# Kernel tuning notes

Measured on AMD Instinct MI355X. Metric: run time of the kernel, lower is better.

The kernel has to match this reference:

```python
import jax, jax.numpy as jnp
import numpy as np

# LIFParameters(thr=0.4, tau=20.0, tau_o=20.0, damp=0.3, n_ref=5)
THR = 0.4
DECAY = float(np.exp(-1.0 / 20.0))   # membrane decay
KAPPA = float(np.exp(-1.0 / 20.0))   # output filter decay
N_REF = 5.0
DAMP = 0.3
SCALE = 1.0                           # scaling_factor

B, NIN, H, NOUT = 1024, 2048, 2048, 512


def setup_inputs() -> dict:
    key = jax.random.key(0)
    ks = jax.random.split(key, 10)
    inputs = (jax.random.uniform(ks[0], (B, NIN)) < 0.1).astype(jnp.float32)   # input spikes
    v = jax.random.uniform(ks[1], (B, H)) * THR                                # membrane potentials
    z = (jax.random.uniform(ks[2], (B, H)) < 0.2).astype(jnp.float32)          # previous spikes
    r = jax.random.randint(ks[3], (B, H), 0, 6).astype(jnp.float32)            # refractory counters
    out = jax.random.normal(ks[4], (B, NOUT)) * 0.1                            # filtered output
    trace_in = jax.random.uniform(ks[5], (B, NIN))
    trace_rec = jax.random.uniform(ks[6], (B, H))
    w_in = jax.random.normal(ks[7], (NIN, H)) / np.sqrt(NIN)
    w_rec = jax.random.normal(ks[8], (H, H)) / np.sqrt(H)
    w_out = jax.random.normal(ks[9], (H, NOUT)) / np.sqrt(H)
    return dict(inputs=inputs, v=v, z=z, r=r, out=out, trace_in=trace_in,
                trace_rec=trace_rec, w_in=w_in, w_rec=w_rec, w_out=w_out)


@jax.custom_vjp
def spike(v_scaled):
    return (v_scaled > 0.0).astype(v_scaled.dtype)

def _spike_fwd(v_scaled):
    return spike(v_scaled), v_scaled

def _spike_bwd(v_scaled, g):
    # surrogate gradient: damp * max(0, 1 - |v_scaled|)
    return (g * DAMP * jnp.maximum(1.0 - jnp.abs(v_scaled), 0.0),)

spike.defvjp(_spike_fwd, _spike_bwd)


def reference(inputs, v, z, r, out, trace_in, trace_rec, w_in, w_rec, w_out):
    # --- lif_step ---
    i_t = inputs @ w_in + z @ w_rec                      # [B,H] synaptic current
    new_v = DECAY * v + i_t - z * THR                    # leaky integration + reset
    v_scaled = (new_v - THR) / THR
    new_z = spike(v_scaled)
    new_z = jnp.where(r > 0.1, 0.0, new_z)               # refractory masking (old r)
    new_r = jnp.clip(r + N_REF * new_z - 1.0, 0.0, N_REF)
    new_out = KAPPA * out + new_z @ (w_out * SCALE)      # [B,NOUT]
    # --- e-prop extras (call_eprop) ---
    dz_dh = jnp.maximum(DAMP * (1.0 - jnp.abs(v_scaled)), 0.0) / THR
    dz_dh = jnp.where(r > 0.1, 0.0, dz_dh)               # zero in refractory period
    new_trace_in = trace_in * DECAY + inputs
    new_trace_rec = trace_rec * DECAY + z
    return (new_out, new_z, new_v, new_r, new_trace_in, new_trace_rec, dz_dh)
```

## Files before the change

### kernel.cpp

```cpp
#include <hip/hip_runtime.h>

#define Bq 1024
#define Hq 2048
#define NOUTq 512

#define DECAYF 0.95122942450071400910f
#define THRF 0.4f

#define OFF_OUT  0
#define OFF_Z    524288
#define OFF_V    2621440
#define OFF_R    4718592
#define OFF_TIN  6815744
#define OFF_TREC 8912896
#define OFF_DZ   11010048

#define WS_ACOMB 0ul
#define WS_WHI   8388608ul
#define WS_WLO   25165824ul
#define WS_WOUTT 41943040ul
#define WS_P     44040192ul
#define WS_Z2    77594624ul
#define WS_NEED  81788928ul

typedef __attribute__((ext_vector_type(8))) short  bf16x8;
typedef __attribute__((ext_vector_type(4))) short  s16x4;
typedef __attribute__((ext_vector_type(4))) float  f32x4;

__device__ __forceinline__ unsigned short cvt_bf16(float f) {
  unsigned u = __float_as_uint(f);
  return (unsigned short)((u + 0x7FFFu + ((u >> 16) & 1u)) >> 16);
}

__device__ __forceinline__ void gl_lds16(const void* g, void* l) {
  __builtin_amdgcn_global_load_lds((const __attribute__((address_space(1))) unsigned int*)g,
                                   (__attribute__((address_space(3))) unsigned int*)l, 16, 0, 0);
}


__global__ __launch_bounds__(256)
void trace_convA(const f32x4* __restrict__ tin, const f32x4* __restrict__ ins,
                 const f32x4* __restrict__ trec, const f32x4* __restrict__ zin,
                 f32x4* __restrict__ o1, f32x4* __restrict__ o2, short* __restrict__ Acomb)
{
  const int i = blockIdx.x * 256 + threadIdx.x;
  const f32x4 b = ins[i];
  const f32x4 d = zin[i];
  o1[i] = tin[i] * DECAYF + b;
  o2[i] = trec[i] * DECAYF + d;
  const int e = i * 4, m = e >> 11, k = e & 2047;
  s16x4 ab, zb;
#pragma unroll
  for (int j = 0; j < 4; ++j) { ab[j] = (short)cvt_bf16(b[j]); zb[j] = (short)cvt_bf16(d[j]); }
  *(s16x4*)&Acomb[m * 4096 + k] = ab;
  *(s16x4*)&Acomb[m * 4096 + 2048 + k] = zb;
}

__global__ __launch_bounds__(256)
void convW(const float* __restrict__ w_in, const float* __restrict__ w_rec,
           const float* __restrict__ w_out, short* __restrict__ Whi,
           short* __restrict__ Wlo, short* __restrict__ WoutT)
{
  __shared__ float tile[64][65];
  const int tid = threadIdx.x;
  const int rr = tid >> 4, c4 = (tid & 15) * 4;
  const int bx = blockIdx.x;
  if (bx < 2048) {
    const int k0 = (bx >> 5) * 64, n0 = (bx & 31) * 64;
#pragma unroll
    for (int p = 0; p < 4; ++p) {
      const int kk = p * 16 + rr, kg = k0 + kk;
      const float* src = (kg < 2048) ? &w_in[kg * 2048 + n0 + c4]
                                     : &w_rec[(kg - 2048) * 2048 + n0 + c4];
      const f32x4 v = *(const f32x4*)src;
#pragma unroll
      for (int j = 0; j < 4; ++j) tile[kk][c4 + j] = v[j];
    }
    __syncthreads();
#pragma unroll
    for (int p = 0; p < 4; ++p) {
      const int nn = p * 16 + rr;
      s16x4 hh, ll;
#pragma unroll
      for (int j = 0; j < 4; ++j) {
        const float w = tile[c4 + j][nn];
        const unsigned short h = cvt_bf16(w);
        hh[j] = (short)h;
        ll[j] = (short)cvt_bf16(w - __uint_as_float(((unsigned)h) << 16));
      }
      *(s16x4*)&Whi[(n0 + nn) * 4096 + k0 + c4] = hh;
      *(s16x4*)&Wlo[(n0 + nn) * 4096 + k0 + c4] = ll;
    }
  } else {
    const int b2 = bx - 2048;
    const int k0 = (b2 >> 3) * 64, n0 = (b2 & 7) * 64;
#pragma unroll
    for (int p = 0; p < 4; ++p) {
      const int kk = p * 16 + rr;
      const f32x4 v = *(const f32x4*)&w_out[(k0 + kk) * 512 + n0 + c4];
#pragma unroll
      for (int j = 0; j < 4; ++j) tile[kk][c4 + j] = v[j];
    }
    __syncthreads();
#pragma unroll
    for (int p = 0; p < 4; ++p) {
      const int nn = p * 16 + rr;
      s16x4 hh;
#pragma unroll
      for (int j = 0; j < 4; ++j) hh[j] = (short)cvt_bf16(tile[c4 + j][nn]);
      *(s16x4*)&WoutT[(n0 + nn) * 2048 + k0 + c4] = hh;
    }
  }
}

template<int MODE>
__global__ __launch_bounds__(256, 1)
void gemm_lds(const short* __restrict__ Ag, const short* __restrict__ Whg,
              const short* __restrict__ Wlg, const float* __restrict__ e0,
              float* __restrict__ outp)
{
  constexpr int BM  = MODE == 0 ? 128 : 32;
  constexpr int BN  = MODE == 0 ? 128 : 64;
  constexpr int MR  = MODE == 0 ? 4 : 1;
  constexpr int NR  = MODE == 0 ? 4 : 2;
  constexpr int KT  = MODE == 0 ? 16 : 32;
  constexpr int AK  = MODE == 0 ? 4096 : 2048;
  constexpr int APW = BM / 32;
  constexpr int WPW = BN / 32;

  __shared__ __align__(16) short As[BM * 64];
  __shared__ __align__(16) short Wh[BN * 64];
  __shared__ __align__(16) short Wl[MODE == 0 ? BN * 64 : 8];

  const int tid = threadIdx.x, lane = tid & 63, wv = tid >> 6;
  const int lr = lane & 15, hl = lane >> 4;
  const int rA = lane >> 3, ts = lane & 7;

  int m0, n0, kz;
  if constexpr (MODE == 0) {
    const int bid = blockIdx.x;
    const int swz = (bid & 7) * 64 + (bid >> 3);
    m0 = (swz & 7) * BM;
    n0 = ((swz >> 3) & 15) * BN;
    kz = swz >> 7;
  } else {
    m0 = blockIdx.y * BM; n0 = blockIdx.x * BN; kz = 0;
  }
  const int kb = kz * 1024;
  float* P = (MODE == 0) ? outp + (size_t)kz * (Bq * Hq) : outp;

  const int wm = (wv >> 1) * (MR * 16);
  const int wn = (wv & 1) * (NR * 16);

  f32x4 acc[MR][NR];
#pragma unroll
  for (int mi = 0; mi < MR; ++mi)
#pragma unroll
    for (int ni = 0; ni < NR; ++ni) acc[mi][ni] = (f32x4){0.f, 0.f, 0.f, 0.f};

  auto STAGE = [&](int kt) {
    const int k = kb + kt * 64;
#pragma unroll
    for (int q = 0; q < APW; ++q) {
      const int slot = wv * APW + q;
      const int r = slot * 8 + rA;
      const int s = ts ^ (r & 7);
      gl_lds16(Ag + (m0 + r) * AK + k + s * 8, &As[slot * 512]);
    }
#pragma unroll
    for (int q = 0; q < WPW; ++q) {
      const int slot = wv * WPW + q;
      const int r = slot * 8 + rA;
      const int s = ts ^ (r & 7);
      gl_lds16(Whg + (n0 + r) * AK + k + s * 8, &Wh[slot * 512]);
      if constexpr (MODE == 0)
        gl_lds16(Wlg + (n0 + r) * AK + k + s * 8, &Wl[slot * 512]);
    }
  };

  STAGE(0);
  for (int kt = 0; kt < KT; ++kt) {
    __syncthreads();
#pragma unroll
    for (int ks = 0; ks < 2; ++ks) {
      bf16x8 af[MR];
#pragma unroll
      for (int mi = 0; mi < MR; ++mi) {
        const int r = wm + mi * 16 + lr;
        af[mi] = *(const bf16x8*)&As[r * 64 + (((ks * 4 + hl) ^ (r & 7)) << 3)];
      }
#pragma unroll
      for (int ni = 0; ni < NR; ++ni) {
        const int rn = wn + ni * 16 + lr;
        const int sp = (((ks * 4 + hl) ^ (rn & 7)) << 3);
        const bf16x8 bh = *(const bf16x8*)&Wh[rn * 64 + sp];
#pragma unroll
        for (int mi = 0; mi < MR; ++mi)
          acc[mi][ni] = __builtin_amdgcn_mfma_f32_16x16x32_bf16(af[mi], bh, acc[mi][ni], 0, 0, 0);
        if constexpr (MODE == 0) {
          const bf16x8 bl = *(const bf16x8*)&Wl[rn * 64 + sp];
#pragma unroll
          for (int mi = 0; mi < MR; ++mi)
            acc[mi][ni] = __builtin_amdgcn_mfma_f32_16x16x32_bf16(af[mi], bl, acc[mi][ni], 0, 0, 0);
        }
      }
    }
    __syncthreads();
    if (kt + 1 < KT) STAGE(kt + 1);
  }

#pragma unroll
  for (int mi = 0; mi < MR; ++mi)
#pragma unroll
    for (int ni = 0; ni < NR; ++ni)
#pragma unroll
      for (int j = 0; j < 4; ++j) {
        const int m = m0 + wm + mi * 16 + hl * 4 + j;
        const int n = n0 + wn + ni * 16 + lr;
        if constexpr (MODE == 0) {
          P[m * Hq + n] = acc[mi][ni][j];
        } else {
          const int idx = m * NOUTq + n;
          outp[idx] = DECAYF * e0[idx] + acc[mi][ni][j];
        }
      }
}

__global__ __launch_bounds__(256)
void lif_epi(const f32x4* __restrict__ Pp, const f32x4* __restrict__ vin,
             const f32x4* __restrict__ zin, const f32x4* __restrict__ rin,
             float* __restrict__ dout, short* __restrict__ z2)
{
  const int i = blockIdx.x * 256 + threadIdx.x;
  const f32x4 it = Pp[i] + Pp[i + 524288] + Pp[i + 2 * 524288] + Pp[i + 3 * 524288];
  const f32x4 vo = vin[i], zo = zin[i], ro = rin[i];
  f32x4 nv, nz, nr, dz;
  s16x4 zb;
#pragma unroll
  for (int j = 0; j < 4; ++j) {
    const float v1 = DECAYF * vo[j] + it[j] - zo[j] * THRF;
    const float vs = (v1 - THRF) / THRF;
    const bool refr = ro[j] > 0.1f;
    const float z1 = (refr || !(vs > 0.0f)) ? 0.0f : 1.0f;
    nv[j] = v1; nz[j] = z1;
    nr[j] = fminf(fmaxf(ro[j] + 5.0f * z1 - 1.0f, 0.0f), 5.0f);
    dz[j] = refr ? 0.0f : (fmaxf(0.3f * (1.0f - fabsf(vs)), 0.0f) / THRF);
    zb[j] = (short)cvt_bf16(z1);
  }
  ((f32x4*)(dout + OFF_V))[i] = nv;
  ((f32x4*)(dout + OFF_Z))[i] = nz;
  ((f32x4*)(dout + OFF_R))[i] = nr;
  ((f32x4*)(dout + OFF_DZ))[i] = dz;
  ((s16x4*)z2)[i] = zb;
}


template<int MODE>
__global__ __launch_bounds__(256, 1)
void fb_gemm(const float* __restrict__ A0g, const float* __restrict__ A1g,
             const float* __restrict__ W0g, const float* __restrict__ W1g,
             const float* __restrict__ e0, const float* __restrict__ e1,
             const float* __restrict__ e2, float* __restrict__ dout)
{
  constexpr int BM = (MODE == 0) ? 64 : 32;
  constexpr int BN = (MODE == 0) ? 128 : 64;
  constexpr int BK = 64;
  constexpr int LDA = BK + 8;
  constexpr int MR = (MODE == 0) ? 2 : 1;
  constexpr int NR = (MODE == 0) ? 4 : 2;
  constexpr int WM = MR * 16, WN = NR * 16;
  constexpr int KT = (MODE == 0) ? 64 : 32;
  constexpr int Nmat = (MODE == 0) ? Hq : NOUTq;
  constexpr int QA = BM / 16;
  constexpr int QW = (16 * BN) / 256;
  constexpr int KSH = (MODE == 0) ? 7 : 6;
  constexpr int KSTEP = (MODE == 0) ? 2 : 4;

  __shared__ __align__(16) short As[BM * LDA];
  __shared__ __align__(16) short Wh[BN * LDA];
  __shared__ __align__(16) short Wl[((MODE == 0) ? BN : 1) * LDA];

  const int tid  = threadIdx.x;
  const int lane = tid & 63;
  const int wave = tid >> 6;
  const int lr = lane & 15, hl = lane >> 4;
  const int wmOff = (wave >> 1) * WM;
  const int wnOff = (wave & 1) * WN;
  const int m0 = blockIdx.y * BM;
  const int n0 = blockIdx.x * BN;
  const int arow = tid >> 4, ac4 = tid & 15;
  const int wn = tid & (BN - 1);

  f32x4 aR[QA];
  float wR[QW][4];
  f32x4 acc[MR][NR];
#pragma unroll
  for (int mi = 0; mi < MR; ++mi)
#pragma unroll
    for (int ni = 0; ni < NR; ++ni)
      acc[mi][ni] = (f32x4){0.f, 0.f, 0.f, 0.f};

  auto LOAD = [&](int kt) {
    const float* Ag = A0g; const float* Wg = W0g; int k0 = kt * BK;
    if (MODE == 0 && kt >= 32) { Ag = A1g; Wg = W1g; k0 = (kt - 32) * BK; }
#pragma unroll
    for (int q = 0; q < QA; ++q)
      aR[q] = *(const f32x4*)&Ag[(m0 + arow + q * 16) * 2048 + k0 + ac4 * 4];
#pragma unroll
    for (int p = 0; p < QW; ++p) {
      const int kq = (tid >> KSH) + p * KSTEP;
#pragma unroll
      for (int i = 0; i < 4; ++i)
        wR[p][i] = Wg[(k0 + kq * 4 + i) * Nmat + n0 + wn];
    }
  };

  auto STORE = [&]() {
#pragma unroll
    for (int q = 0; q < QA; ++q) {
      s16x4 hv;
#pragma unroll
      for (int j = 0; j < 4; ++j) hv[j] = (short)cvt_bf16(aR[q][j]);
      *(s16x4*)&As[(arow + q * 16) * LDA + ac4 * 4] = hv;
    }
#pragma unroll
    for (int p = 0; p < QW; ++p) {
      const int kq = (tid >> KSH) + p * KSTEP;
      s16x4 hh, ll;
#pragma unroll
      for (int i = 0; i < 4; ++i) {
        const float w = wR[p][i];
        const unsigned short h = cvt_bf16(w);
        hh[i] = (short)h;
        if (MODE == 0) {
          const float hf = __uint_as_float(((unsigned)h) << 16);
          ll[i] = (short)cvt_bf16(w - hf);
        }
      }
      *(s16x4*)&Wh[wn * LDA + kq * 4] = hh;
      if (MODE == 0) *(s16x4*)&Wl[wn * LDA + kq * 4] = ll;
    }
  };

  LOAD(0);
  for (int kt = 0; kt < KT; ++kt) {
    __syncthreads();
    STORE();
    __syncthreads();
    if (kt + 1 < KT) LOAD(kt + 1);
#pragma unroll
    for (int ks = 0; ks < 2; ++ks) {
      bf16x8 af[MR];
#pragma unroll
      for (int mi = 0; mi < MR; ++mi)
        af[mi] = *(const bf16x8*)&As[(wmOff + mi * 16 + lr) * LDA + ks * 32 + hl * 8];
#pragma unroll
      for (int ni = 0; ni < NR; ++ni) {
        const bf16x8 bh = *(const bf16x8*)&Wh[(wnOff + ni * 16 + lr) * LDA + ks * 32 + hl * 8];
#pragma unroll
        for (int mi = 0; mi < MR; ++mi)
          acc[mi][ni] = __builtin_amdgcn_mfma_f32_16x16x32_bf16(af[mi], bh, acc[mi][ni], 0, 0, 0);
        if (MODE == 0) {
          const bf16x8 bl = *(const bf16x8*)&Wl[(wnOff + ni * 16 + lr) * LDA + ks * 32 + hl * 8];
#pragma unroll
          for (int mi = 0; mi < MR; ++mi)
            acc[mi][ni] = __builtin_amdgcn_mfma_f32_16x16x32_bf16(af[mi], bl, acc[mi][ni], 0, 0, 0);
        }
      }
    }
  }

#pragma unroll
  for (int mi = 0; mi < MR; ++mi) {
#pragma unroll
    for (int ni = 0; ni < NR; ++ni) {
#pragma unroll
      for (int j = 0; j < 4; ++j) {
        const int m = m0 + wmOff + mi * 16 + hl * 4 + j;
        const int n = n0 + wnOff + ni * 16 + lr;
        if (MODE == 0) {
          const int idx = m * Hq + n;
          const float it = acc[mi][ni][j];
          const float vold = e0[idx];
          const float zold = e1[idx];
          const float rold = e2[idx];
          const float nv = DECAYF * vold + it - zold * THRF;
          const float vs = (nv - THRF) / THRF;
          const bool refr = rold > 0.1f;
          const float nz = (refr || !(vs > 0.0f)) ? 0.0f : 1.0f;
          const float nr = fminf(fmaxf(rold + 5.0f * nz - 1.0f, 0.0f), 5.0f);
          const float dz = refr ? 0.0f : (fmaxf(0.3f * (1.0f - fabsf(vs)), 0.0f) / THRF);
          dout[OFF_V + idx] = nv;
          dout[OFF_Z + idx] = nz;
          dout[OFF_R + idx] = nr;
          dout[OFF_DZ + idx] = dz;
        } else {
          const int idx = m * NOUTq + n;
          dout[OFF_OUT + idx] = DECAYF * e0[idx] + acc[mi][ni][j];
        }
      }
    }
  }
}

__global__ __launch_bounds__(256)
void fb_trace(const float4* __restrict__ tin, const float4* __restrict__ ins,
              const float4* __restrict__ trec, const float4* __restrict__ zin,
              float4* __restrict__ o1, float4* __restrict__ o2)
{
  const int n4 = (Bq * 2048) / 4;
  for (int i = blockIdx.x * blockDim.x + threadIdx.x; i < n4; i += gridDim.x * blockDim.x) {
    const float4 a = tin[i], b = ins[i];
    float4 u;
    u.x = a.x * DECAYF + b.x; u.y = a.y * DECAYF + b.y;
    u.z = a.z * DECAYF + b.z; u.w = a.w * DECAYF + b.w;
    o1[i] = u;
    const float4 c = trec[i], d = zin[i];
    float4 w;
    w.x = c.x * DECAYF + d.x; w.y = c.y * DECAYF + d.y;
    w.z = c.z * DECAYF + d.z; w.w = c.w * DECAYF + d.w;
    o2[i] = w;
  }
}

extern "C" void kernel_launch(void* const* d_in, const int* in_sizes, int n_in,
                              void* d_out, int out_size, void* d_ws, size_t ws_size,
                              hipStream_t stream) {
  const float* inputs = (const float*)d_in[0];
  const float* v      = (const float*)d_in[1];
  const float* z      = (const float*)d_in[2];
  const float* r      = (const float*)d_in[3];
  const float* outp   = (const float*)d_in[4];
  const float* tin    = (const float*)d_in[5];
  const float* trec   = (const float*)d_in[6];
  const float* w_in   = (const float*)d_in[7];
  const float* w_rec  = (const float*)d_in[8];
  const float* w_out  = (const float*)d_in[9];
  float* out = (float*)d_out;

  if (ws_size >= WS_NEED) {
    char* ws = (char*)d_ws;
    short* Acomb = (short*)(ws + WS_ACOMB);
    short* Whi   = (short*)(ws + WS_WHI);
    short* Wlo   = (short*)(ws + WS_WLO);
    short* WoutT = (short*)(ws + WS_WOUTT);
    float* P     = (float*)(ws + WS_P);
    short* Z2    = (short*)(ws + WS_Z2);

    trace_convA<<<2048, 256, 0, stream>>>((const f32x4*)tin, (const f32x4*)inputs,
                                          (const f32x4*)trec, (const f32x4*)z,
                                          (f32x4*)(out + OFF_TIN), (f32x4*)(out + OFF_TREC), Acomb);
    convW<<<2304, 256, 0, stream>>>(w_in, w_rec, w_out, Whi, Wlo, WoutT);
    gemm_lds<0><<<512, 256, 0, stream>>>(Acomb, Whi, Wlo, nullptr, P);
    lif_epi<<<2048, 256, 0, stream>>>((const f32x4*)P, (const f32x4*)v, (const f32x4*)z,
                                      (const f32x4*)r, out, Z2);
    gemm_lds<1><<<dim3(8, 32), 256, 0, stream>>>(Z2, WoutT, nullptr, outp, out + OFF_OUT);
  } else {
    fb_trace<<<2048, 256, 0, stream>>>((const float4*)tin, (const float4*)inputs,
                                       (const float4*)trec, (const float4*)z,
                                       (float4*)(out + OFF_TIN), (float4*)(out + OFF_TREC));
    fb_gemm<0><<<dim3(16, 16), 256, 0, stream>>>(inputs, z, w_in, w_rec, v, z, r, out);
    fb_gemm<1><<<dim3(8, 32), 256, 0, stream>>>(out + OFF_Z, nullptr, w_out, nullptr,
                                                outp, nullptr, nullptr, out);
  }
}
```

Measured before the change: 93.63 us.

## Fuse prep kernels and fold LIF epilogue into split-K GEMM via counters

Merges the trace/activation conversion and weight conversion kernels into one launch. Folds the LIF epilogue into the split-K GEMM: each tile increments an atomic counter, and the last of the four K-slices to finish reduces the partials and applies the LIF update. This removes one kernel launch and the separate full pass that re-read the partials. In exchange it adds a memset, threadfences and atomics, and the epilogue work runs only in the last-arriving blocks, which can leave a tail.

```diff
diff --git a/kernel.cpp b/kernel.cpp
--- a/kernel.cpp
+++ b/kernel.cpp
@@ -21,7 +21,8 @@
 #define WS_WOUTT 41943040ul
 #define WS_P     44040192ul
 #define WS_Z2    77594624ul
-#define WS_NEED  81788928ul
+#define WS_CNT   81788928ul
+#define WS_NEED  81793024ul
 
 typedef __attribute__((ext_vector_type(8))) short  bf16x8;
 typedef __attribute__((ext_vector_type(4))) short  s16x4;
@@ -39,34 +40,33 @@
 
 
 __global__ __launch_bounds__(256)
-void trace_convA(const f32x4* __restrict__ tin, const f32x4* __restrict__ ins,
-                 const f32x4* __restrict__ trec, const f32x4* __restrict__ zin,
-                 f32x4* __restrict__ o1, f32x4* __restrict__ o2, short* __restrict__ Acomb)
-{
-  const int i = blockIdx.x * 256 + threadIdx.x;
-  const f32x4 b = ins[i];
-  const f32x4 d = zin[i];
-  o1[i] = tin[i] * DECAYF + b;
-  o2[i] = trec[i] * DECAYF + d;
-  const int e = i * 4, m = e >> 11, k = e & 2047;
-  s16x4 ab, zb;
-#pragma unroll
-  for (int j = 0; j < 4; ++j) { ab[j] = (short)cvt_bf16(b[j]); zb[j] = (short)cvt_bf16(d[j]); }
-  *(s16x4*)&Acomb[m * 4096 + k] = ab;
-  *(s16x4*)&Acomb[m * 4096 + 2048 + k] = zb;
-}
-
-__global__ __launch_bounds__(256)
-void convW(const float* __restrict__ w_in, const float* __restrict__ w_rec,
-           const float* __restrict__ w_out, short* __restrict__ Whi,
-           short* __restrict__ Wlo, short* __restrict__ WoutT)
+void prep(const f32x4* __restrict__ tin, const f32x4* __restrict__ ins,
+          const f32x4* __restrict__ trec, const f32x4* __restrict__ zin,
+          f32x4* __restrict__ o1, f32x4* __restrict__ o2, short* __restrict__ Acomb,
+          const float* __restrict__ w_in, const float* __restrict__ w_rec,
+          const float* __restrict__ w_out, short* __restrict__ Whi,
+          short* __restrict__ Wlo, short* __restrict__ WoutT)
 {
   __shared__ float tile[64][65];
-  const int tid = threadIdx.x;
+  const int bx = blockIdx.x, tid = threadIdx.x;
+  if (bx < 2048) {
+    const int i = bx * 256 + tid;
+    const f32x4 b = ins[i];
+    const f32x4 d = zin[i];
+    o1[i] = tin[i] * DECAYF + b;
+    o2[i] = trec[i] * DECAYF + d;
+    const int e = i * 4, m = e >> 11, k = e & 2047;
+    s16x4 ab, zb;
+#pragma unroll
+    for (int j = 0; j < 4; ++j) { ab[j] = (short)cvt_bf16(b[j]); zb[j] = (short)cvt_bf16(d[j]); }
+    *(s16x4*)&Acomb[m * 4096 + k] = ab;
+    *(s16x4*)&Acomb[m * 4096 + 2048 + k] = zb;
+    return;
+  }
   const int rr = tid >> 4, c4 = (tid & 15) * 4;
-  const int bx = blockIdx.x;
-  if (bx < 2048) {
-    const int k0 = (bx >> 5) * 64, n0 = (bx & 31) * 64;
+  if (bx < 4096) {
+    const int bxx = bx - 2048;
+    const int k0 = (bxx >> 5) * 64, n0 = (bxx & 31) * 64;
 #pragma unroll
     for (int p = 0; p < 4; ++p) {
       const int kk = p * 16 + rr, kg = k0 + kk;
@@ -92,7 +92,7 @@
       *(s16x4*)&Wlo[(n0 + nn) * 4096 + k0 + c4] = ll;
     }
   } else {
-    const int b2 = bx - 2048;
+    const int b2 = bx - 4096;
     const int k0 = (b2 >> 3) * 64, n0 = (b2 & 7) * 64;
 #pragma unroll
     for (int p = 0; p < 4; ++p) {
@@ -117,7 +117,9 @@
 __global__ __launch_bounds__(256, 1)
 void gemm_lds(const short* __restrict__ Ag, const short* __restrict__ Whg,
               const short* __restrict__ Wlg, const float* __restrict__ e0,
-              float* __restrict__ outp)
+              float* outp, unsigned* cnt,
+              const f32x4* __restrict__ vin, const f32x4* __restrict__ zin,
+              const f32x4* __restrict__ rin, float* dout, short* z2)
 {
   constexpr int BM  = MODE == 0 ? 128 : 32;
   constexpr int BN  = MODE == 0 ? 128 : 64;
@@ -131,6 +133,7 @@
   __shared__ __align__(16) short As[BM * 64];
   __shared__ __align__(16) short Wh[BN * 64];
   __shared__ __align__(16) short Wl[MODE == 0 ? BN * 64 : 8];
+  __shared__ unsigned sFin;
 
   const int tid = threadIdx.x, lane = tid & 63, wv = tid >> 6;
   const int lr = lane & 15, hl = lane >> 4;
@@ -224,34 +227,42 @@
           outp[idx] = DECAYF * e0[idx] + acc[mi][ni][j];
         }
       }
-}
-
-__global__ __launch_bounds__(256)
-void lif_epi(const f32x4* __restrict__ Pp, const f32x4* __restrict__ vin,
-             const f32x4* __restrict__ zin, const f32x4* __restrict__ rin,
-             float* __restrict__ dout, short* __restrict__ z2)
-{
-  const int i = blockIdx.x * 256 + threadIdx.x;
-  const f32x4 it = Pp[i] + Pp[i + 524288] + Pp[i + 2 * 524288] + Pp[i + 3 * 524288];
-  const f32x4 vo = vin[i], zo = zin[i], ro = rin[i];
-  f32x4 nv, nz, nr, dz;
-  s16x4 zb;
-#pragma unroll
-  for (int j = 0; j < 4; ++j) {
-    const float v1 = DECAYF * vo[j] + it[j] - zo[j] * THRF;
-    const float vs = (v1 - THRF) / THRF;
-    const bool refr = ro[j] > 0.1f;
-    const float z1 = (refr || !(vs > 0.0f)) ? 0.0f : 1.0f;
-    nv[j] = v1; nz[j] = z1;
-    nr[j] = fminf(fmaxf(ro[j] + 5.0f * z1 - 1.0f, 0.0f), 5.0f);
-    dz[j] = refr ? 0.0f : (fmaxf(0.3f * (1.0f - fabsf(vs)), 0.0f) / THRF);
-    zb[j] = (short)cvt_bf16(z1);
-  }
-  ((f32x4*)(dout + OFF_V))[i] = nv;
-  ((f32x4*)(dout + OFF_Z))[i] = nz;
-  ((f32x4*)(dout + OFF_R))[i] = nr;
-  ((f32x4*)(dout + OFF_DZ))[i] = dz;
-  ((s16x4*)z2)[i] = zb;
+
+  if constexpr (MODE == 0) {
+    __threadfence();
+    const int tileId = (m0 >> 7) * 16 + (n0 >> 7);
+    if (tid == 0) sFin = atomicAdd(cnt + tileId, 1u);
+    __syncthreads();
+    if (sFin == 3u) {
+      __threadfence();
+      const f32x4* P4 = (const f32x4*)outp;
+      const int row4 = n0 >> 2;
+      for (int q = tid; q < (BM * BN) / 4; q += 256) {
+        const int row = q >> 5, c4i = q & 31;
+        const int g4 = (m0 + row) * (Hq / 4) + row4 + c4i;
+        const f32x4 it = P4[g4] + P4[g4 + 524288] + P4[g4 + 2 * 524288] + P4[g4 + 3 * 524288];
+        const f32x4 vo = vin[g4], zo = zin[g4], ro = rin[g4];
+        f32x4 nv, nz, nr, dz;
+        s16x4 zb;
+#pragma unroll
+        for (int j = 0; j < 4; ++j) {
+          const float v1 = DECAYF * vo[j] + it[j] - zo[j] * THRF;
+          const float vs = (v1 - THRF) / THRF;
+          const bool refr = ro[j] > 0.1f;
+          const float z1 = (refr || !(vs > 0.0f)) ? 0.0f : 1.0f;
+          nv[j] = v1; nz[j] = z1;
+          nr[j] = fminf(fmaxf(ro[j] + 5.0f * z1 - 1.0f, 0.0f), 5.0f);
+          dz[j] = refr ? 0.0f : (fmaxf(0.3f * (1.0f - fabsf(vs)), 0.0f) / THRF);
+          zb[j] = (short)cvt_bf16(z1);
+        }
+        ((f32x4*)(dout + OFF_V))[g4] = nv;
+        ((f32x4*)(dout + OFF_Z))[g4] = nz;
+        ((f32x4*)(dout + OFF_R))[g4] = nr;
+        ((f32x4*)(dout + OFF_DZ))[g4] = dz;
+        ((s16x4*)z2)[g4] = zb;
+      }
+    }
+  }
 }
 
 
@@ -446,15 +457,19 @@
     short* WoutT = (short*)(ws + WS_WOUTT);
     float* P     = (float*)(ws + WS_P);
     short* Z2    = (short*)(ws + WS_Z2);
-
-    trace_convA<<<2048, 256, 0, stream>>>((const f32x4*)tin, (const f32x4*)inputs,
-                                          (const f32x4*)trec, (const f32x4*)z,
-                                          (f32x4*)(out + OFF_TIN), (f32x4*)(out + OFF_TREC), Acomb);
-    convW<<<2304, 256, 0, stream>>>(w_in, w_rec, w_out, Whi, Wlo, WoutT);
-    gemm_lds<0><<<512, 256, 0, stream>>>(Acomb, Whi, Wlo, nullptr, P);
-    lif_epi<<<2048, 256, 0, stream>>>((const f32x4*)P, (const f32x4*)v, (const f32x4*)z,
-                                      (const f32x4*)r, out, Z2);
-    gemm_lds<1><<<dim3(8, 32), 256, 0, stream>>>(Z2, WoutT, nullptr, outp, out + OFF_OUT);
+    unsigned* C  = (unsigned*)(ws + WS_CNT);
+
+    hipMemsetAsync(C, 0, 512, stream);
+    prep<<<4352, 256, 0, stream>>>((const f32x4*)tin, (const f32x4*)inputs,
+                                   (const f32x4*)trec, (const f32x4*)z,
+                                   (f32x4*)(out + OFF_TIN), (f32x4*)(out + OFF_TREC), Acomb,
+                                   w_in, w_rec, w_out, Whi, Wlo, WoutT);
+    gemm_lds<0><<<512, 256, 0, stream>>>(Acomb, Whi, Wlo, nullptr, P, C,
+                                         (const f32x4*)v, (const f32x4*)z, (const f32x4*)r,
+                                         out, Z2);
+    gemm_lds<1><<<dim3(8, 32), 256, 0, stream>>>(Z2, WoutT, nullptr, outp, out + OFF_OUT,
+                                                 nullptr, nullptr, nullptr, nullptr,
+                                                 nullptr, nullptr);
   } else {
     fb_trace<<<2048, 256, 0, stream>>>((const float4*)tin, (const float4*)inputs,
                                        (const float4*)trec, (const float4*)z,
```

Result: slower. 218.2 us (+133.1%).

## Merge prep kernels and retile main GEMM to 128x64 with split-K of two

Applied to the files above, without the earlier changes.

Merges the trace/A-conversion kernel and the weight conversion kernel into a single prep launch that dispatches on block index, removing one kernel launch and its tail. The main GEMM now uses 128x64 tiles with a 2-way K split instead of 128x128 tiles with a 4-way split, still with 512 blocks. That halves the partial-sum buffer traffic the LIF epilogue reads and writes. The trade-off is less register-level reuse per block and longer K loops per block.

```diff
diff --git a/kernel.cpp b/kernel.cpp
--- a/kernel.cpp
+++ b/kernel.cpp
@@ -39,34 +39,33 @@
 
 
 __global__ __launch_bounds__(256)
-void trace_convA(const f32x4* __restrict__ tin, const f32x4* __restrict__ ins,
-                 const f32x4* __restrict__ trec, const f32x4* __restrict__ zin,
-                 f32x4* __restrict__ o1, f32x4* __restrict__ o2, short* __restrict__ Acomb)
-{
-  const int i = blockIdx.x * 256 + threadIdx.x;
-  const f32x4 b = ins[i];
-  const f32x4 d = zin[i];
-  o1[i] = tin[i] * DECAYF + b;
-  o2[i] = trec[i] * DECAYF + d;
-  const int e = i * 4, m = e >> 11, k = e & 2047;
-  s16x4 ab, zb;
-#pragma unroll
-  for (int j = 0; j < 4; ++j) { ab[j] = (short)cvt_bf16(b[j]); zb[j] = (short)cvt_bf16(d[j]); }
-  *(s16x4*)&Acomb[m * 4096 + k] = ab;
-  *(s16x4*)&Acomb[m * 4096 + 2048 + k] = zb;
-}
-
-__global__ __launch_bounds__(256)
-void convW(const float* __restrict__ w_in, const float* __restrict__ w_rec,
-           const float* __restrict__ w_out, short* __restrict__ Whi,
-           short* __restrict__ Wlo, short* __restrict__ WoutT)
+void prep(const f32x4* __restrict__ tin, const f32x4* __restrict__ ins,
+          const f32x4* __restrict__ trec, const f32x4* __restrict__ zin,
+          f32x4* __restrict__ o1, f32x4* __restrict__ o2, short* __restrict__ Acomb,
+          const float* __restrict__ w_in, const float* __restrict__ w_rec,
+          const float* __restrict__ w_out, short* __restrict__ Whi,
+          short* __restrict__ Wlo, short* __restrict__ WoutT)
 {
   __shared__ float tile[64][65];
-  const int tid = threadIdx.x;
+  const int bx = blockIdx.x, tid = threadIdx.x;
+  if (bx < 2048) {
+    const int i = bx * 256 + tid;
+    const f32x4 b = ins[i];
+    const f32x4 d = zin[i];
+    o1[i] = tin[i] * DECAYF + b;
+    o2[i] = trec[i] * DECAYF + d;
+    const int e = i * 4, m = e >> 11, k = e & 2047;
+    s16x4 ab, zb;
+#pragma unroll
+    for (int j = 0; j < 4; ++j) { ab[j] = (short)cvt_bf16(b[j]); zb[j] = (short)cvt_bf16(d[j]); }
+    *(s16x4*)&Acomb[m * 4096 + k] = ab;
+    *(s16x4*)&Acomb[m * 4096 + 2048 + k] = zb;
+    return;
+  }
   const int rr = tid >> 4, c4 = (tid & 15) * 4;
-  const int bx = blockIdx.x;
-  if (bx < 2048) {
-    const int k0 = (bx >> 5) * 64, n0 = (bx & 31) * 64;
+  if (bx < 4096) {
+    const int bxx = bx - 2048;
+    const int k0 = (bxx >> 5) * 64, n0 = (bxx & 31) * 64;
 #pragma unroll
     for (int p = 0; p < 4; ++p) {
       const int kk = p * 16 + rr, kg = k0 + kk;
@@ -92,7 +91,7 @@
       *(s16x4*)&Wlo[(n0 + nn) * 4096 + k0 + c4] = ll;
     }
   } else {
-    const int b2 = bx - 2048;
+    const int b2 = bx - 4096;
     const int k0 = (b2 >> 3) * 64, n0 = (b2 & 7) * 64;
 #pragma unroll
     for (int p = 0; p < 4; ++p) {
@@ -120,10 +119,10 @@
               float* __restrict__ outp)
 {
   constexpr int BM  = MODE == 0 ? 128 : 32;
-  constexpr int BN  = MODE == 0 ? 128 : 64;
+  constexpr int BN  = 64;
   constexpr int MR  = MODE == 0 ? 4 : 1;
-  constexpr int NR  = MODE == 0 ? 4 : 2;
-  constexpr int KT  = MODE == 0 ? 16 : 32;
+  constexpr int NR  = 2;
+  constexpr int KT  = 32;
   constexpr int AK  = MODE == 0 ? 4096 : 2048;
   constexpr int APW = BM / 32;
   constexpr int WPW = BN / 32;
@@ -141,12 +140,12 @@
     const int bid = blockIdx.x;
     const int swz = (bid & 7) * 64 + (bid >> 3);
     m0 = (swz & 7) * BM;
-    n0 = ((swz >> 3) & 15) * BN;
-    kz = swz >> 7;
+    n0 = ((swz >> 3) & 31) * BN;
+    kz = swz >> 8;
   } else {
     m0 = blockIdx.y * BM; n0 = blockIdx.x * BN; kz = 0;
   }
-  const int kb = kz * 1024;
+  const int kb = kz * 2048;
   float* P = (MODE == 0) ? outp + (size_t)kz * (Bq * Hq) : outp;
 
   const int wm = (wv >> 1) * (MR * 16);
@@ -232,7 +231,7 @@
              float* __restrict__ dout, short* __restrict__ z2)
 {
   const int i = blockIdx.x * 256 + threadIdx.x;
-  const f32x4 it = Pp[i] + Pp[i + 524288] + Pp[i + 2 * 524288] + Pp[i + 3 * 524288];
+  const f32x4 it = Pp[i] + Pp[i + 524288];
   const f32x4 vo = vin[i], zo = zin[i], ro = rin[i];
   f32x4 nv, nz, nr, dz;
   s16x4 zb;
@@ -447,10 +446,10 @@
     float* P     = (float*)(ws + WS_P);
     short* Z2    = (short*)(ws + WS_Z2);
 
-    trace_convA<<<2048, 256, 0, stream>>>((const f32x4*)tin, (const f32x4*)inputs,
-                                          (const f32x4*)trec, (const f32x4*)z,
-                                          (f32x4*)(out + OFF_TIN), (f32x4*)(out + OFF_TREC), Acomb);
-    convW<<<2304, 256, 0, stream>>>(w_in, w_rec, w_out, Whi, Wlo, WoutT);
+    prep<<<4352, 256, 0, stream>>>((const f32x4*)tin, (const f32x4*)inputs,
+                                   (const f32x4*)trec, (const f32x4*)z,
+                                   (f32x4*)(out + OFF_TIN), (f32x4*)(out + OFF_TREC), Acomb,
+                                   w_in, w_rec, w_out, Whi, Wlo, WoutT);
     gemm_lds<0><<<512, 256, 0, stream>>>(Acomb, Whi, Wlo, nullptr, P);
     lif_epi<<<2048, 256, 0, stream>>>((const f32x4*)P, (const f32x4*)v, (const f32x4*)z,
                                       (const f32x4*)r, out, Z2);
```

After: 92.97 us. About the same (-0.7%).

## Merge activation conversion into weight prep and trace updates into output GEMM

Applied to the files above, without the earlier changes.

Folds the bf16 conversion of inputs and z into the weight-conversion kernel as extra blocks. It also moves the trace_in/trace_rec decay updates into the final output GEMM launch as extra blocks. This removes one launch and lets the elementwise trace work run alongside the small, under-occupied output GEMM instead of serially at the start. The trade-off is that the tail kernel loses the launch_bounds(256,1) hint, and block scheduling order may delay the GEMM blocks.

```diff
diff --git a/kernel.cpp b/kernel.cpp
--- a/kernel.cpp
+++ b/kernel.cpp
@@ -39,32 +39,27 @@
 
 
 __global__ __launch_bounds__(256)
-void trace_convA(const f32x4* __restrict__ tin, const f32x4* __restrict__ ins,
-                 const f32x4* __restrict__ trec, const f32x4* __restrict__ zin,
-                 f32x4* __restrict__ o1, f32x4* __restrict__ o2, short* __restrict__ Acomb)
-{
-  const int i = blockIdx.x * 256 + threadIdx.x;
-  const f32x4 b = ins[i];
-  const f32x4 d = zin[i];
-  o1[i] = tin[i] * DECAYF + b;
-  o2[i] = trec[i] * DECAYF + d;
-  const int e = i * 4, m = e >> 11, k = e & 2047;
-  s16x4 ab, zb;
-#pragma unroll
-  for (int j = 0; j < 4; ++j) { ab[j] = (short)cvt_bf16(b[j]); zb[j] = (short)cvt_bf16(d[j]); }
-  *(s16x4*)&Acomb[m * 4096 + k] = ab;
-  *(s16x4*)&Acomb[m * 4096 + 2048 + k] = zb;
-}
-
-__global__ __launch_bounds__(256)
-void convW(const float* __restrict__ w_in, const float* __restrict__ w_rec,
-           const float* __restrict__ w_out, short* __restrict__ Whi,
-           short* __restrict__ Wlo, short* __restrict__ WoutT)
+void prepWA(const float* __restrict__ w_in, const float* __restrict__ w_rec,
+            const float* __restrict__ w_out, short* __restrict__ Whi,
+            short* __restrict__ Wlo, short* __restrict__ WoutT,
+            const f32x4* __restrict__ ins, const f32x4* __restrict__ zin,
+            short* __restrict__ Acomb)
 {
   __shared__ float tile[64][65];
-  const int tid = threadIdx.x;
+  const int bx = blockIdx.x, tid = threadIdx.x;
+  if (bx >= 2304) {
+    const int i = (bx - 2304) * 256 + tid;
+    const f32x4 b = ins[i];
+    const f32x4 d = zin[i];
+    const int e = i * 4, m = e >> 11, k = e & 2047;
+    s16x4 ab, zb;
+#pragma unroll
+    for (int j = 0; j < 4; ++j) { ab[j] = (short)cvt_bf16(b[j]); zb[j] = (short)cvt_bf16(d[j]); }
+    *(s16x4*)&Acomb[m * 4096 + k] = ab;
+    *(s16x4*)&Acomb[m * 4096 + 2048 + k] = zb;
+    return;
+  }
   const int rr = tid >> 4, c4 = (tid & 15) * 4;
-  const int bx = blockIdx.x;
   if (bx < 2048) {
     const int k0 = (bx >> 5) * 64, n0 = (bx & 31) * 64;
 #pragma unroll
@@ -113,41 +108,28 @@
   }
 }
 
-template<int MODE>
 __global__ __launch_bounds__(256, 1)
-void gemm_lds(const short* __restrict__ Ag, const short* __restrict__ Whg,
-              const short* __restrict__ Wlg, const float* __restrict__ e0,
-              float* __restrict__ outp)
+void gemm1(const short* __restrict__ Ag, const short* __restrict__ Whg,
+           const short* __restrict__ Wlg, float* __restrict__ outp)
 {
-  constexpr int BM  = MODE == 0 ? 128 : 32;
-  constexpr int BN  = MODE == 0 ? 128 : 64;
-  constexpr int MR  = MODE == 0 ? 4 : 1;
-  constexpr int NR  = MODE == 0 ? 4 : 2;
-  constexpr int KT  = MODE == 0 ? 16 : 32;
-  constexpr int AK  = MODE == 0 ? 4096 : 2048;
-  constexpr int APW = BM / 32;
-  constexpr int WPW = BN / 32;
+  constexpr int BM = 128, BN = 128, MR = 4, NR = 4, KT = 16, AK = 4096;
+  constexpr int APW = BM / 32, WPW = BN / 32;
 
   __shared__ __align__(16) short As[BM * 64];
   __shared__ __align__(16) short Wh[BN * 64];
-  __shared__ __align__(16) short Wl[MODE == 0 ? BN * 64 : 8];
+  __shared__ __align__(16) short Wl[BN * 64];
 
   const int tid = threadIdx.x, lane = tid & 63, wv = tid >> 6;
   const int lr = lane & 15, hl = lane >> 4;
   const int rA = lane >> 3, ts = lane & 7;
 
-  int m0, n0, kz;
-  if constexpr (MODE == 0) {
-    const int bid = blockIdx.x;
-    const int swz = (bid & 7) * 64 + (bid >> 3);
-    m0 = (swz & 7) * BM;
-    n0 = ((swz >> 3) & 15) * BN;
-    kz = swz >> 7;
-  } else {
-    m0 = blockIdx.y * BM; n0 = blockIdx.x * BN; kz = 0;
-  }
+  const int bid = blockIdx.x;
+  const int swz = (bid & 7) * 64 + (bid >> 3);
+  const int m0 = (swz & 7) * BM;
+  const int n0 = ((swz >> 3) & 15) * BN;
+  const int kz = swz >> 7;
   const int kb = kz * 1024;
-  float* P = (MODE == 0) ? outp + (size_t)kz * (Bq * Hq) : outp;
+  float* P = outp + (size_t)kz * (Bq * Hq);
 
   const int wm = (wv >> 1) * (MR * 16);
   const int wn = (wv & 1) * (NR * 16);
@@ -173,8 +155,7 @@
       const int r = slot * 8 + rA;
       const int s = ts ^ (r & 7);
       gl_lds16(Whg + (n0 + r) * AK + k + s * 8, &Wh[slot * 512]);
-      if constexpr (MODE == 0)
-        gl_lds16(Wlg + (n0 + r) * AK + k + s * 8, &Wl[slot * 512]);
+      gl_lds16(Wlg + (n0 + r) * AK + k + s * 8, &Wl[slot * 512]);
     }
   };
 
@@ -197,12 +178,10 @@
 #pragma unroll
         for (int mi = 0; mi < MR; ++mi)
           acc[mi][ni] = __builtin_amdgcn_mfma_f32_16x16x32_bf16(af[mi], bh, acc[mi][ni], 0, 0, 0);
-        if constexpr (MODE == 0) {
-          const bf16x8 bl = *(const bf16x8*)&Wl[rn * 64 + sp];
-#pragma unroll
-          for (int mi = 0; mi < MR; ++mi)
-            acc[mi][ni] = __builtin_amdgcn_mfma_f32_16x16x32_bf16(af[mi], bl, acc[mi][ni], 0, 0, 0);
-        }
+        const bf16x8 bl = *(const bf16x8*)&Wl[rn * 64 + sp];
+#pragma unroll
+        for (int mi = 0; mi < MR; ++mi)
+          acc[mi][ni] = __builtin_amdgcn_mfma_f32_16x16x32_bf16(af[mi], bl, acc[mi][ni], 0, 0, 0);
       }
     }
     __syncthreads();
@@ -217,12 +196,7 @@
       for (int j = 0; j < 4; ++j) {
         const int m = m0 + wm + mi * 16 + hl * 4 + j;
         const int n = n0 + wn + ni * 16 + lr;
-        if constexpr (MODE == 0) {
-          P[m * Hq + n] = acc[mi][ni][j];
-        } else {
-          const int idx = m * NOUTq + n;
-          outp[idx] = DECAYF * e0[idx] + acc[mi][ni][j];
-        }
+        P[m * Hq + n] = acc[mi][ni][j];
       }
 }
 
@@ -252,6 +226,94 @@
   ((f32x4*)(dout + OFF_R))[i] = nr;
   ((f32x4*)(dout + OFF_DZ))[i] = dz;
   ((s16x4*)z2)[i] = zb;
+}
+
+__global__ __launch_bounds__(256)
+void tail(const short* __restrict__ Ag, const short* __restrict__ Whg,
+          const float* __restrict__ e0, float* __restrict__ outp,
+          const f32x4* __restrict__ tin, const f32x4* __restrict__ ins,
+          const f32x4* __restrict__ trec, const f32x4* __restrict__ zin,
+          f32x4* __restrict__ o1, f32x4* __restrict__ o2)
+{
+  constexpr int BM = 32, BN = 64, MR = 1, NR = 2, KT = 32, AK = 2048;
+  constexpr int APW = BM / 32, WPW = BN / 32;
+  __shared__ __align__(16) short As[BM * 64];
+  __shared__ __align__(16) short Wh[BN * 64];
+
+  const int bid = blockIdx.x, tid = threadIdx.x;
+  if (bid >= 256) {
+    const int i = (bid - 256) * 256 + tid;
+    o1[i] = tin[i] * DECAYF + ins[i];
+    o2[i] = trec[i] * DECAYF + zin[i];
+    return;
+  }
+  const int lane = tid & 63, wv = tid >> 6;
+  const int lr = lane & 15, hl = lane >> 4;
+  const int rA = lane >> 3, ts = lane & 7;
+  const int m0 = (bid >> 3) * BM, n0 = (bid & 7) * BN;
+  const int wm = (wv >> 1) * (MR * 16);
+  const int wn = (wv & 1) * (NR * 16);
+
+  f32x4 acc[MR][NR];
+#pragma unroll
+  for (int mi = 0; mi < MR; ++mi)
+#pragma unroll
+    for (int ni = 0; ni < NR; ++ni) acc[mi][ni] = (f32x4){0.f, 0.f, 0.f, 0.f};
+
+  auto STAGE = [&](int kt) {
+    const int k = kt * 64;
+#pragma unroll
+    for (int q = 0; q < APW; ++q) {
+      const int slot = wv * APW + q;
+      const int r = slot * 8 + rA;
+      const int s = ts ^ (r & 7);
+      gl_lds16(Ag + (m0 + r) * AK + k + s * 8, &As[slot * 512]);
+    }
+#pragma unroll
+    for (int q = 0; q < WPW; ++q) {
+      const int slot = wv * WPW + q;
+      const int r = slot * 8 + rA;
+      const int s = ts ^ (r & 7);
+      gl_lds16(Whg + (n0 + r) * AK + k + s * 8, &Wh[slot * 512]);
+    }
+  };
+
+  STAGE(0);
+  for (int kt = 0; kt < KT; ++kt) {
+    __syncthreads();
+#pragma unroll
+    for (int ks = 0; ks < 2; ++ks) {
+      bf16x8 af[MR];
+#pragma unroll
+      for (int mi = 0; mi < MR; ++mi) {
+        const int r = wm + mi * 16 + lr;
+        af[mi] = *(const bf16x8*)&As[r * 64 + (((ks * 4 + hl) ^ (r & 7)) << 3)];
+      }
+#pragma unroll
+      for (int ni = 0; ni < NR; ++ni) {
+        const int rn = wn + ni * 16 + lr;
+        const int sp = (((ks * 4 + hl) ^ (rn & 7)) << 3);
+        const bf16x8 bh = *(const bf16x8*)&Wh[rn * 64 + sp];
+#pragma unroll
+        for (int mi = 0; mi < MR; ++mi)
+          acc[mi][ni] = __builtin_amdgcn_mfma_f32_16x16x32_bf16(af[mi], bh, acc[mi][ni], 0, 0, 0);
+      }
+    }
+    __syncthreads();
+    if (kt + 1 < KT) STAGE(kt + 1);
+  }
+
+#pragma unroll
+  for (int mi = 0; mi < MR; ++mi)
+#pragma unroll
+    for (int ni = 0; ni < NR; ++ni)
+#pragma unroll
+      for (int j = 0; j < 4; ++j) {
+        const int m = m0 + wm + mi * 16 + hl * 4 + j;
+        const int n = n0 + wn + ni * 16 + lr;
+        const int idx = m * NOUTq + n;
+        outp[idx] = DECAYF * e0[idx] + acc[mi][ni][j];
+      }
 }
 
 
@@ -447,14 +509,15 @@
     float* P     = (float*)(ws + WS_P);
     short* Z2    = (short*)(ws + WS_Z2);
 
-    trace_convA<<<2048, 256, 0, stream>>>((const f32x4*)tin, (const f32x4*)inputs,
-                                          (const f32x4*)trec, (const f32x4*)z,
-                                          (f32x4*)(out + OFF_TIN), (f32x4*)(out + OFF_TREC), Acomb);
-    convW<<<2304, 256, 0, stream>>>(w_in, w_rec, w_out, Whi, Wlo, WoutT);
-    gemm_lds<0><<<512, 256, 0, stream>>>(Acomb, Whi, Wlo, nullptr, P);
+    prepWA<<<4352, 256, 0, stream>>>(w_in, w_rec, w_out, Whi, Wlo, WoutT,
+                                     (const f32x4*)inputs, (const f32x4*)z, Acomb);
+    gemm1<<<512, 256, 0, stream>>>(Acomb, Whi, Wlo, P);
     lif_epi<<<2048, 256, 0, stream>>>((const f32x4*)P, (const f32x4*)v, (const f32x4*)z,
                                       (const f32x4*)r, out, Z2);
-    gemm_lds<1><<<dim3(8, 32), 256, 0, stream>>>(Z2, WoutT, nullptr, outp, out + OFF_OUT);
+    tail<<<2304, 256, 0, stream>>>(Z2, WoutT, outp, out + OFF_OUT,
+                                   (const f32x4*)tin, (const f32x4*)inputs,
+                                   (const f32x4*)trec, (const f32x4*)z,
+                                   (f32x4*)(out + OFF_TIN), (f32x4*)(out + OFF_TREC));
   } else {
     fb_trace<<<2048, 256, 0, stream>>>((const float4*)tin, (const float4*)inputs,
                                        (const float4*)trec, (const float4*)z,
```

After: 91.23 us. 1.03x faster.
